# Kernel tuning notes

Hardware: AMD Instinct MI355X
Metric: run time of the kernel (lower is better)

Reference implementation:

```python
import jax, jax.numpy as jnp
import numpy as np

K, D, B = 512, 64, 4096  # n_primitives, view_dim, batch
TRIL_I, TRIL_J = np.tril_indices(D, -1)  # matches torch.tril_indices(D, D, offset=-1)
EPS = 1e-8


def setup_inputs() -> dict:
    key = jax.random.key(0)
    k1, k2, k3 = jax.random.split(key, 3)
    z = jax.random.normal(k1, (B, D), dtype=jnp.float32)
    # _init_weights: mu ~ N(0, 1/sqrt(D)) (random_normal mode)
    mu = jax.random.normal(k2, (K, D), dtype=jnp.float32) / np.float32(np.sqrt(D))
    # log_diag = 2*log(precision_init_scale) = 0 for scale=1, no jitter
    log_diag = jnp.zeros((K, D), dtype=jnp.float32)
    # point_softmax mode -> log_s zero-init
    log_s = jnp.zeros((K,), dtype=jnp.float32)
    # full covariance: lower_offdiag ~ N(0, offdiag_init_std=0.01)
    lower_offdiag = 0.01 * jax.random.normal(k3, (K, D * (D - 1) // 2), dtype=jnp.float32)
    return {"z": z, "mu": mu, "log_diag": log_diag, "log_s": log_s,
            "lower_offdiag": lower_offdiag}


def _precision_cholesky(log_diag, lower_offdiag):
    # (K, D, D) lower-triangular Cholesky factor of the precision matrix
    chol = jnp.zeros((K, D, D), dtype=log_diag.dtype)
    didx = jnp.arange(D)
    chol = chol.at[:, didx, didx].set(jnp.exp(0.5 * log_diag))
    chol = chol.at[:, TRIL_I, TRIL_J].set(lower_offdiag)
    return chol


def reference(z, mu, log_diag, log_s, lower_offdiag):
    chol = _precision_cholesky(log_diag, lower_offdiag)          # (K, D, D)
    diff = z[:, None, :] - mu[None, :, :]                        # (B, K, D)
    transformed = jnp.einsum('bkd,kde->bke', diff, chol)         # (B, K, D)
    mahal = jnp.sum(transformed * transformed, axis=-1)          # (B, K)
    strength = jax.nn.softplus(log_s)                            # (K,)
    log_a = -0.5 * mahal + jnp.log(strength + EPS)[None, :]
    log_a_max = jax.lax.stop_gradient(jnp.max(log_a, axis=-1, keepdims=True))
    a = jnp.exp(log_a - log_a_max)
    alpha = a / (jnp.sum(a, axis=-1, keepdims=True) + EPS)       # (B, K)
    return alpha
```

## Files before the change

kernel.cpp:

```cpp
#include <hip/hip_runtime.h>
#include <hip/hip_bf16.h>
#include <math.h>

#define KP   512
#define DD   64
#define BB   4096
#define NTRI 2016

typedef __attribute__((ext_vector_type(8))) short bfrag;
typedef __attribute__((ext_vector_type(4))) float facc4;


__device__ __forceinline__ void async16(const void* g, void* l) {
    __builtin_amdgcn_global_load_lds(
        (const __attribute__((address_space(1))) unsigned int*)g,
        (__attribute__((address_space(3))) unsigned int*)l, 16, 0, 0);
}

__global__ __launch_bounds__(256) void prep_kernel(
    const float* __restrict__ mu, const float* __restrict__ log_diag,
    const float* __restrict__ log_s, const float* __restrict__ lod,
    unsigned short* __restrict__ Limg, float* __restrict__ wws,
    float* __restrict__ biasws)
{
    const int k = blockIdx.x;
    const int tid = threadIdx.x;
    __shared__ float Lc[64 * 64];
    __shared__ float muS[64];
    __shared__ float wp[4][64];

    for (int idx = tid; idx < 4096; idx += 256) Lc[idx] = 0.0f;
    if (tid < 64) muS[tid] = mu[k * 64 + tid];
    __syncthreads();

    if (tid < 64) Lc[tid * 64 + tid] = expf(0.5f * log_diag[k * 64 + tid]);
    for (int t = tid; t < NTRI; t += 256) {
        int i = (int)((1.0f + sqrtf(8.0f * (float)t + 1.0f)) * 0.5f);
        while (i * (i - 1) / 2 > t) --i;
        while ((i + 1) * i / 2 <= t) ++i;
        int j = t - i * (i - 1) / 2;
        Lc[j * 64 + i] = lod[(size_t)k * NTRI + t];
    }
    __syncthreads();

    {
        const int e = tid & 63, part = tid >> 6;
        float s = 0.0f;
        for (int d = e + part; d < 64; d += 4)
            s += muS[d] * Lc[e * 64 + d];
        wp[part][e] = s;
    }
    __syncthreads();
    if (tid < 64)
        wws[k * 64 + tid] = -(wp[0][tid] + wp[1][tid] + wp[2][tid] + wp[3][tid]);

    for (int idx = tid; idx < 4096; idx += 256) {
        int e = idx >> 6, d = idx & 63;
        int sw = (e << 6) | (d ^ ((e & 7) << 3));
        __hip_bfloat16 hb = __float2bfloat16(Lc[idx]);
        Limg[(size_t)k * 4096 + sw] = *(unsigned short*)&hb;
    }
    if (tid == 0) {
        float s = log_s[k];
        float sp = (s > 20.0f) ? s : log1pf(expf(s));
        biasws[k] = logf(sp + 1e-8f);
    }
}

__global__ __launch_bounds__(256) void mahal_kernel(
    const float* __restrict__ z, const unsigned short* __restrict__ Limg,
    const float* __restrict__ wws, float* __restrict__ mahal)
{
    __shared__ __align__(16) char  ldsImg[4][8192];
    __shared__ __align__(16) float wS[16 * 64];

    const int tid  = threadIdx.x;
    const int wave = tid >> 6;
    const int lane = tid & 63;
    const int g    = lane >> 4;
    const int l15  = lane & 15;

    const int n      = blockIdx.x;
    const int kslice = (n & 7) + ((n >> 8) << 3);
    const int bblk   = (n >> 3) & 31;
    const int k0     = kslice * 16;
    const int bw     = bblk * 128 + wave * 32;

    const char* imgK = (const char*)Limg + (size_t)k0 * 8192;

#pragma unroll
    for (int b0 = 0; b0 < 2; ++b0) {
        const char* src = imgK + (size_t)b0 * 8192;
        char* dst = &ldsImg[b0][0];
#pragma unroll
        for (int p = 0; p < 2; ++p) {
            const int cof = p * 4096 + wave * 1024;
            async16(src + cof + lane * 16, dst + cof);
        }
    }

    for (int i = tid; i < 16 * 64; i += 256) wS[i] = wws[k0 * 64 + i];

    bfrag zh[2][2], zl[2][2];
#pragma unroll
    for (int bs = 0; bs < 2; ++bs) {
        const float* zp = z + (size_t)(bw + bs * 16 + l15) * 64 + 8 * g;
#pragma unroll
        for (int ds = 0; ds < 2; ++ds) {
            float4 a = *(const float4*)(zp + ds * 32);
            float4 c = *(const float4*)(zp + ds * 32 + 4);
            float vv[8] = {a.x, a.y, a.z, a.w, c.x, c.y, c.z, c.w};
            bfrag th, tl;
#pragma unroll
            for (int j = 0; j < 8; ++j) {
                __hip_bfloat16 hb = __float2bfloat16(vv[j]);
                float hv = __bfloat162float(hb);
                __hip_bfloat16 lb = __float2bfloat16(vv[j] - hv);
                th[j] = *(short*)&hb;
                tl[j] = *(short*)&lb;
            }
            zh[bs][ds] = th;
            zl[bs][ds] = tl;
        }
    }

    const int swz = (l15 & 7) << 4;

    __syncthreads();

    for (int t = 0; t < 16; ++t) {
        if (t + 2 < 16) {
            const char* src = imgK + (size_t)(t + 2) * 8192;
            char* dst = &ldsImg[(t + 2) & 3][0];
#pragma unroll
            for (int p = 0; p < 2; ++p) {
                const int cof = p * 4096 + wave * 1024;
                async16(src + cof + lane * 16, dst + cof);
            }
        }

        if (t < 14)       asm volatile("s_waitcnt vmcnt(8)" ::: "memory");
        else if (t == 14) asm volatile("s_waitcnt vmcnt(6)" ::: "memory");
        else              asm volatile("s_waitcnt vmcnt(4)" ::: "memory");
        __builtin_amdgcn_s_barrier();

        const char* buf = &ldsImg[t & 3][0];

        const float* wrow = wS + t * 64;
        facc4 wv[4];
#pragma unroll
        for (int et = 0; et < 4; ++et)
            wv[et] = *(const facc4*)(wrow + et * 16 + 4 * g);

        facc4 acc[4][2];

        __builtin_amdgcn_s_setprio(1);
#pragma unroll
        for (int ds = 0; ds < 2; ++ds) {
#pragma unroll
            for (int et = 0; et < 4; ++et) {
                if (et >= 2 && ds == 0) continue;
                const bool first = (ds == 0) ? (et < 2) : (et >= 2);
                const int ao = et * 2048 + l15 * 128 + ((ds * 64 + 16 * g) ^ swz);
                bfrag lh = *(const bfrag*)(buf + ao);
#pragma unroll
                for (int bs = 0; bs < 2; ++bs) {
                    acc[et][bs] = __builtin_amdgcn_mfma_f32_16x16x32_bf16(
                        lh, zh[bs][ds], first ? wv[et] : acc[et][bs], 0, 0, 0);
                    acc[et][bs] = __builtin_amdgcn_mfma_f32_16x16x32_bf16(
                        lh, zl[bs][ds], acc[et][bs], 0, 0, 0);
                }
            }
        }
        __builtin_amdgcn_s_setprio(0);

        const int k = k0 + t;
#pragma unroll
        for (int bs = 0; bs < 2; ++bs) {
            float p0 = 0.f, p1 = 0.f, p2 = 0.f, p3 = 0.f;
#pragma unroll
            for (int et = 0; et < 4; ++et) {
                p0 = fmaf(acc[et][bs][0], acc[et][bs][0], p0);
                p1 = fmaf(acc[et][bs][1], acc[et][bs][1], p1);
                p2 = fmaf(acc[et][bs][2], acc[et][bs][2], p2);
                p3 = fmaf(acc[et][bs][3], acc[et][bs][3], p3);
            }
            float s = (p0 + p1) + (p2 + p3);
            s += __shfl_xor(s, 16, 64);
            s += __shfl_xor(s, 32, 64);
            if (g == 0)
                mahal[(size_t)(bw + bs * 16 + l15) * KP + k] = s;
        }
    }
}

__global__ __launch_bounds__(256) void softmax_kernel(
    const float* __restrict__ mahal, const float* __restrict__ biasws,
    float* __restrict__ alpha)
{
    const int tid  = threadIdx.x;
    const int lane = tid & 63;
    const int b    = blockIdx.x * 4 + (tid >> 6);

    const float* mrow = mahal + (size_t)b * KP + lane * 8;
    const float* brow = biasws + lane * 8;
    float4 m0 = *(const float4*)(mrow);
    float4 m1 = *(const float4*)(mrow + 4);
    float4 c0 = *(const float4*)(brow);
    float4 c1 = *(const float4*)(brow + 4);

    float la[8];
    la[0] = fmaf(-0.5f, m0.x, c0.x); la[1] = fmaf(-0.5f, m0.y, c0.y);
    la[2] = fmaf(-0.5f, m0.z, c0.z); la[3] = fmaf(-0.5f, m0.w, c0.w);
    la[4] = fmaf(-0.5f, m1.x, c1.x); la[5] = fmaf(-0.5f, m1.y, c1.y);
    la[6] = fmaf(-0.5f, m1.z, c1.z); la[7] = fmaf(-0.5f, m1.w, c1.w);

    float lm = la[0];
#pragma unroll
    for (int j = 1; j < 8; ++j) lm = fmaxf(lm, la[j]);
#pragma unroll
    for (int off = 32; off >= 1; off >>= 1)
        lm = fmaxf(lm, __shfl_xor(lm, off, 64));

    float a[8], s = 0.0f;
#pragma unroll
    for (int j = 0; j < 8; ++j) { a[j] = expf(la[j] - lm); s += a[j]; }
#pragma unroll
    for (int off = 32; off >= 1; off >>= 1)
        s += __shfl_xor(s, off, 64);

    const float r = 1.0f / (s + 1e-8f);
    float4 o0 = {a[0] * r, a[1] * r, a[2] * r, a[3] * r};
    float4 o1 = {a[4] * r, a[5] * r, a[6] * r, a[7] * r};
    float* orow = alpha + (size_t)b * KP + lane * 8;
    *(float4*)(orow)     = o0;
    *(float4*)(orow + 4) = o1;
}

extern "C" void kernel_launch(void* const* d_in, const int* in_sizes, int n_in,
                              void* d_out, int out_size, void* d_ws, size_t ws_size,
                              hipStream_t stream) {
    const float* z        = (const float*)d_in[0];
    const float* mu       = (const float*)d_in[1];
    const float* log_diag = (const float*)d_in[2];
    const float* log_s    = (const float*)d_in[3];
    const float* lod      = (const float*)d_in[4];
    float* out = (float*)d_out;

    char* ws = (char*)d_ws;
    unsigned short* Limg = (unsigned short*)ws;
    float* wws    = (float*)(ws + (size_t)KP * 8192);
    float* biasws = wws + (size_t)KP * 64;
    float* mahalws = biasws + KP;

    prep_kernel<<<KP, 256, 0, stream>>>(mu, log_diag, log_s, lod, Limg, wws, biasws);
    mahal_kernel<<<1024, 256, 0, stream>>>(z, Limg, wws, mahalws);
    softmax_kernel<<<BB / 4, 256, 0, stream>>>(mahalws, biasws, out);
}
```

Before: 46.64 us.

## Switch mahal GEMM to 32x32x16 MFMA tiles with triangular skipping

```diff
diff --git a/kernel.cpp b/kernel.cpp
--- a/kernel.cpp
+++ b/kernel.cpp
@@ -7,8 +7,8 @@
 #define BB   4096
 #define NTRI 2016
 
-typedef __attribute__((ext_vector_type(8))) short bfrag;
-typedef __attribute__((ext_vector_type(4))) float facc4;
+typedef __attribute__((ext_vector_type(8)))  short bfrag;
+typedef __attribute__((ext_vector_type(16))) float facc16;
 
 
 __device__ __forceinline__ void async16(const void* g, void* l) {
@@ -77,8 +77,8 @@
     const int tid  = threadIdx.x;
     const int wave = tid >> 6;
     const int lane = tid & 63;
-    const int g    = lane >> 4;
-    const int l15  = lane & 15;
+    const int h    = lane >> 5;
+    const int l31  = lane & 31;
 
     const int n      = blockIdx.x;
     const int kslice = (n & 7) + ((n >> 8) << 3);
@@ -89,26 +89,22 @@
     const char* imgK = (const char*)Limg + (size_t)k0 * 8192;
 
 #pragma unroll
-    for (int b0 = 0; b0 < 2; ++b0) {
-        const char* src = imgK + (size_t)b0 * 8192;
-        char* dst = &ldsImg[b0][0];
+    for (int b0 = 0; b0 < 2; ++b0)
 #pragma unroll
         for (int p = 0; p < 2; ++p) {
             const int cof = p * 4096 + wave * 1024;
-            async16(src + cof + lane * 16, dst + cof);
-        }
-    }
+            async16(imgK + b0 * 8192 + cof + lane * 16, &ldsImg[b0][0] + cof);
+        }
 
     for (int i = tid; i < 16 * 64; i += 256) wS[i] = wws[k0 * 64 + i];
 
-    bfrag zh[2][2], zl[2][2];
-#pragma unroll
-    for (int bs = 0; bs < 2; ++bs) {
-        const float* zp = z + (size_t)(bw + bs * 16 + l15) * 64 + 8 * g;
-#pragma unroll
-        for (int ds = 0; ds < 2; ++ds) {
-            float4 a = *(const float4*)(zp + ds * 32);
-            float4 c = *(const float4*)(zp + ds * 32 + 4);
+    bfrag zh[4], zl[4];
+    {
+        const float* zp = z + (size_t)(bw + l31) * 64 + 8 * h;
+#pragma unroll
+        for (int ds4 = 0; ds4 < 4; ++ds4) {
+            float4 a = *(const float4*)(zp + ds4 * 16);
+            float4 c = *(const float4*)(zp + ds4 * 16 + 4);
             float vv[8] = {a.x, a.y, a.z, a.w, c.x, c.y, c.z, c.w};
             bfrag th, tl;
 #pragma unroll
@@ -119,12 +115,13 @@
                 th[j] = *(short*)&hb;
                 tl[j] = *(short*)&lb;
             }
-            zh[bs][ds] = th;
-            zl[bs][ds] = tl;
-        }
-    }
-
-    const int swz = (l15 & 7) << 4;
+            zh[ds4] = th;
+            zl[ds4] = tl;
+        }
+    }
+
+    const int swz  = (l31 & 7) << 4;
+    const int rowb = l31 * 128;
 
     __syncthreads();
 
@@ -139,58 +136,72 @@
             }
         }
 
-        if (t < 14)       asm volatile("s_waitcnt vmcnt(8)" ::: "memory");
-        else if (t == 14) asm volatile("s_waitcnt vmcnt(6)" ::: "memory");
-        else              asm volatile("s_waitcnt vmcnt(4)" ::: "memory");
+        if (t < 14)       asm volatile("s_waitcnt vmcnt(6)" ::: "memory");
+        else if (t == 14) asm volatile("s_waitcnt vmcnt(4)" ::: "memory");
+        else              asm volatile("s_waitcnt vmcnt(2)" ::: "memory");
         __builtin_amdgcn_s_barrier();
 
         const char* buf = &ldsImg[t & 3][0];
-
         const float* wrow = wS + t * 64;
-        facc4 wv[4];
-#pragma unroll
-        for (int et = 0; et < 4; ++et)
-            wv[et] = *(const facc4*)(wrow + et * 16 + 4 * g);
-
-        facc4 acc[4][2];
+
+        facc16 ci0;
+#pragma unroll
+        for (int q = 0; q < 4; ++q) {
+            float4 v = *(const float4*)(wrow + q * 8 + 4 * h);
+            ci0[4 * q + 0] = v.x; ci0[4 * q + 1] = v.y;
+            ci0[4 * q + 2] = v.z; ci0[4 * q + 3] = v.w;
+        }
+
+        facc16 acc0, acc1;
 
         __builtin_amdgcn_s_setprio(1);
-#pragma unroll
-        for (int ds = 0; ds < 2; ++ds) {
-#pragma unroll
-            for (int et = 0; et < 4; ++et) {
-                if (et >= 2 && ds == 0) continue;
-                const bool first = (ds == 0) ? (et < 2) : (et >= 2);
-                const int ao = et * 2048 + l15 * 128 + ((ds * 64 + 16 * g) ^ swz);
-                bfrag lh = *(const bfrag*)(buf + ao);
-#pragma unroll
-                for (int bs = 0; bs < 2; ++bs) {
-                    acc[et][bs] = __builtin_amdgcn_mfma_f32_16x16x32_bf16(
-                        lh, zh[bs][ds], first ? wv[et] : acc[et][bs], 0, 0, 0);
-                    acc[et][bs] = __builtin_amdgcn_mfma_f32_16x16x32_bf16(
-                        lh, zl[bs][ds], acc[et][bs], 0, 0, 0);
-                }
-            }
+        {
+            bfrag f = *(const bfrag*)(buf + rowb + ((16 * h) ^ swz));
+            acc0 = __builtin_amdgcn_mfma_f32_32x32x16_bf16(f, zh[0], ci0, 0, 0, 0);
+            acc0 = __builtin_amdgcn_mfma_f32_32x32x16_bf16(f, zl[0], acc0, 0, 0, 0);
+            f = *(const bfrag*)(buf + rowb + ((32 + 16 * h) ^ swz));
+            acc0 = __builtin_amdgcn_mfma_f32_32x32x16_bf16(f, zh[1], acc0, 0, 0, 0);
+            acc0 = __builtin_amdgcn_mfma_f32_32x32x16_bf16(f, zl[1], acc0, 0, 0, 0);
+        }
+        facc16 ci1;
+#pragma unroll
+        for (int q = 0; q < 4; ++q) {
+            float4 v = *(const float4*)(wrow + 32 + q * 8 + 4 * h);
+            ci1[4 * q + 0] = v.x; ci1[4 * q + 1] = v.y;
+            ci1[4 * q + 2] = v.z; ci1[4 * q + 3] = v.w;
+        }
+        {
+            bfrag f = *(const bfrag*)(buf + rowb + ((64 + 16 * h) ^ swz));
+            acc0 = __builtin_amdgcn_mfma_f32_32x32x16_bf16(f, zh[2], acc0, 0, 0, 0);
+            acc0 = __builtin_amdgcn_mfma_f32_32x32x16_bf16(f, zl[2], acc0, 0, 0, 0);
+            f = *(const bfrag*)(buf + 4096 + rowb + ((64 + 16 * h) ^ swz));
+            acc1 = __builtin_amdgcn_mfma_f32_32x32x16_bf16(f, zh[2], ci1, 0, 0, 0);
+            acc1 = __builtin_amdgcn_mfma_f32_32x32x16_bf16(f, zl[2], acc1, 0, 0, 0);
+            f = *(const bfrag*)(buf + rowb + ((96 + 16 * h) ^ swz));
+            acc0 = __builtin_amdgcn_mfma_f32_32x32x16_bf16(f, zh[3], acc0, 0, 0, 0);
+            acc0 = __builtin_amdgcn_mfma_f32_32x32x16_bf16(f, zl[3], acc0, 0, 0, 0);
+            f = *(const bfrag*)(buf + 4096 + rowb + ((96 + 16 * h) ^ swz));
+            acc1 = __builtin_amdgcn_mfma_f32_32x32x16_bf16(f, zh[3], acc1, 0, 0, 0);
+            acc1 = __builtin_amdgcn_mfma_f32_32x32x16_bf16(f, zl[3], acc1, 0, 0, 0);
         }
         __builtin_amdgcn_s_setprio(0);
 
-        const int k = k0 + t;
-#pragma unroll
-        for (int bs = 0; bs < 2; ++bs) {
-            float p0 = 0.f, p1 = 0.f, p2 = 0.f, p3 = 0.f;
-#pragma unroll
-            for (int et = 0; et < 4; ++et) {
-                p0 = fmaf(acc[et][bs][0], acc[et][bs][0], p0);
-                p1 = fmaf(acc[et][bs][1], acc[et][bs][1], p1);
-                p2 = fmaf(acc[et][bs][2], acc[et][bs][2], p2);
-                p3 = fmaf(acc[et][bs][3], acc[et][bs][3], p3);
-            }
-            float s = (p0 + p1) + (p2 + p3);
-            s += __shfl_xor(s, 16, 64);
-            s += __shfl_xor(s, 32, 64);
-            if (g == 0)
-                mahal[(size_t)(bw + bs * 16 + l15) * KP + k] = s;
-        }
+        float p0 = 0.f, p1 = 0.f, p2 = 0.f, p3 = 0.f;
+#pragma unroll
+        for (int r = 0; r < 16; r += 4) {
+            p0 = fmaf(acc0[r + 0], acc0[r + 0], p0);
+            p1 = fmaf(acc0[r + 1], acc0[r + 1], p1);
+            p2 = fmaf(acc0[r + 2], acc0[r + 2], p2);
+            p3 = fmaf(acc0[r + 3], acc0[r + 3], p3);
+            p0 = fmaf(acc1[r + 0], acc1[r + 0], p0);
+            p1 = fmaf(acc1[r + 1], acc1[r + 1], p1);
+            p2 = fmaf(acc1[r + 2], acc1[r + 2], p2);
+            p3 = fmaf(acc1[r + 3], acc1[r + 3], p3);
+        }
+        float s = (p0 + p1) + (p2 + p3);
+        s += __shfl_xor(s, 32, 64);
+        if (h == 0)
+            mahal[(size_t)(bw + l31) * KP + k0 + t] = s;
     }
 }
 
```

After: 48.44 us. 1.04x slower.
